# Kernel tuning notes

Measured on AMD Instinct MI355X. Metric: run time of the kernel, lower is better.

## Reference

```python
import jax, jax.numpy as jnp
import numpy as np

NUM_EMB = 8192
EMB_DIM = 512
SPAN = 8            # max_span == fixed_segment_size
COMMIT = 0.25
BOUND_W = 0.01


def setup_inputs() -> dict:
    key = jax.random.key(0)
    k_x, k_e, k_w = jax.random.split(key, 3)
    B, T, D = 16, 8192, EMB_DIM
    x = jax.random.normal(k_x, (B, T, D), dtype=jnp.float32)
    emb = jax.random.normal(k_e, (NUM_EMB, D), dtype=jnp.float32) * 0.02
    Wb = jax.random.normal(k_w, (D, 1), dtype=jnp.float32) * 0.02
    bb = jnp.zeros((1,), dtype=jnp.float32)
    return {"x": x, "emb": emb, "Wb": Wb, "bb": bb}


def reference(x, emb, Wb, bb):
    # Eval-mode forward of AdaptiveTemporalVQ (no gumbel sampling, no EMA update).
    B, T, D = x.shape
    # boundary predictor: Linear(D, 1) -> squeeze
    boundary_logits = (x @ Wb)[..., 0] + bb[0]                      # [B, T]
    boundaries = (jax.nn.sigmoid(boundary_logits) > 0.5).astype(x.dtype)

    num_segments = (T + SPAN - 1) // SPAN
    pad = num_segments * SPAN - T
    x_p = jnp.pad(x, ((0, 0), (0, pad), (0, 0))) if pad > 0 else x
    # temporal mean pooling over fixed segments
    pooled = x_p.reshape(B, num_segments, SPAN, D).mean(axis=2)      # [B, S, D]

    # --- VectorQuantizer ---
    flat = pooled.reshape(-1, D)                                     # [N, D]
    dist = (jnp.sum(flat ** 2, axis=1, keepdims=True)
            + jnp.sum(emb ** 2, axis=1)
            - 2.0 * flat @ emb.T)                                    # [N, K]
    idx = jnp.argmin(dist, axis=1)                                   # [N]
    quantized = emb[idx].reshape(B, num_segments, D)                 # codebook gather

    e_latent_loss = jnp.mean((jax.lax.stop_gradient(quantized) - pooled) ** 2)
    vq_loss = COMMIT * e_latent_loss
    # straight-through estimator
    q_st = pooled + jax.lax.stop_gradient(quantized - pooled)

    # expand each segment code back over its SPAN timesteps
    q_exp = jnp.broadcast_to(q_st[:, :, None, :], (B, num_segments, SPAN, D))
    quantized_out = q_exp.reshape(B, num_segments * SPAN, D)[:, :T, :]
    idx_seg = idx.reshape(B, num_segments)
    idx_out = jnp.broadcast_to(idx_seg[:, :, None], (B, num_segments, SPAN))
    idx_out = idx_out.reshape(B, num_segments * SPAN)[:, :T]

    target_rate = jnp.float32(1.0 / SPAN)
    boundary_loss = (boundaries.mean() - target_rate) ** 2
    total_loss = vq_loss + BOUND_W * boundary_loss
    return quantized_out, total_loss, idx_out, boundaries
```

## Files before the change

### kernel.cpp

```cpp
#include <hip/hip_runtime.h>

#define B_    16
#define T_    8192
#define D_    512
#define K_    8192
#define S_    1024
#define N_    16384
#define NBT   131072

#define LOSS_OFF 67108864
#define IDX_OFF  67108865
#define BND_OFF  67239937

typedef __bf16 bf16x8 __attribute__((ext_vector_type(8)));
typedef float  f32x4  __attribute__((ext_vector_type(4)));

__device__ __forceinline__ unsigned int fsort(float f){
  unsigned int u = __float_as_uint(f);
  return (u & 0x80000000u) ? ~u : (u | 0x80000000u);
}
__device__ __forceinline__ float funsort(unsigned int su){
  unsigned int u = (su & 0x80000000u) ? (su ^ 0x80000000u) : ~su;
  return __uint_as_float(u);
}
__device__ __forceinline__ unsigned short f2bf(float f){
  unsigned int u = __float_as_uint(f);
  return (unsigned short)((u + 0x7fffu + ((u >> 16) & 1u)) >> 16);
}
__device__ __forceinline__ void gload16(const void* g, void* l){
  __builtin_amdgcn_global_load_lds((const __attribute__((address_space(1))) void*)g,
                                   (__attribute__((address_space(3))) void*)l, 16, 0, 0);
}

#define VMW8()  asm volatile("s_waitcnt vmcnt(8)")
#define VMW4()  asm volatile("s_waitcnt vmcnt(4)")
#define VMW0()  asm volatile("s_waitcnt vmcnt(0)")
#define LGKW()  asm volatile("s_waitcnt lgkmcnt(0)")
#define DSR(dst, addr, OFF) \
  asm volatile("ds_read_b128 %0, %1 offset:" OFF : "=&v"(dst) : "v"(addr))

__global__ void k_embnorm(const float4* __restrict__ emb4, float* __restrict__ enorm,
                          unsigned short* __restrict__ embh, int* __restrict__ cnt){
  if(blockIdx.x == 0 && threadIdx.x == 0) *cnt = 0;
  const int wid  = (blockIdx.x * blockDim.x + threadIdx.x) >> 6;
  const int lane = threadIdx.x & 63;
  float4 a = emb4[wid * 128 + (lane << 1)];
  float4 b = emb4[wid * 128 + (lane << 1) + 1];
  float s = a.x*a.x + a.y*a.y + a.z*a.z + a.w*a.w
          + b.x*b.x + b.y*b.y + b.z*b.z + b.w*b.w;
  #pragma unroll
  for(int off = 32; off; off >>= 1) s += __shfl_xor(s, off);
  if(lane == 0) enorm[wid] = s;
  unsigned short* dst = embh + ((size_t)wid << 9) + (lane << 3);
  *(ushort4*)(dst)     = make_ushort4(f2bf(a.x), f2bf(a.y), f2bf(a.z), f2bf(a.w));
  *(ushort4*)(dst + 4) = make_ushort4(f2bf(b.x), f2bf(b.y), f2bf(b.z), f2bf(b.w));
}

__launch_bounds__(256)
__global__ void k_prep(const float4* __restrict__ x4, const float4* __restrict__ wb4,
                       const float* __restrict__ bb, float4* __restrict__ pooled4,
                       unsigned short* __restrict__ pooledh, float* __restrict__ bnd,
                       int* __restrict__ cnt){
  __shared__ double ld[4][8][8];
  const int tid  = threadIdx.x;
  const int row0 = blockIdx.x << 5;
  const double bbv = (double)bb[0];
  #pragma unroll
  for(int it = 0; it < 2; it++){
    const int slot  = (it << 8) + tid;
    const int seg_l = slot >> 7;
    const int c4    = slot & 127;
    const float4 w  = wb4[c4];
    const float4* src = x4 + ((size_t)(row0 + (seg_l << 3)) * 128 + c4);
    float4 acc = src[0];
    double p[8];
    p[0] = (double)acc.x*w.x + (double)acc.y*w.y + (double)acc.z*w.z + (double)acc.w*w.w;
    #pragma unroll
    for(int t = 1; t < 8; t++){
      const float4 v = src[(size_t)t * 128];
      acc.x += v.x; acc.y += v.y; acc.z += v.z; acc.w += v.w;
      p[t] = (double)v.x*w.x + (double)v.y*w.y + (double)v.z*w.z + (double)v.w*w.w;
    }
    acc.x *= 0.125f; acc.y *= 0.125f; acc.z *= 0.125f; acc.w *= 0.125f;
    const int u = ((blockIdx.x << 2) + seg_l) * 128 + c4;
    pooled4[u] = acc;
    *(ushort4*)(pooledh + ((size_t)u << 2)) =
        make_ushort4(f2bf(acc.x), f2bf(acc.y), f2bf(acc.z), f2bf(acc.w));
    #pragma unroll
    for(int t = 0; t < 8; t++){
      #pragma unroll
      for(int off = 1; off < 16; off <<= 1) p[t] += __shfl_xor(p[t], off);
    }
    if((c4 & 15) == 0){
      #pragma unroll
      for(int t = 0; t < 8; t++) ld[seg_l][t][c4 >> 4] = p[t];
    }
  }
  __syncthreads();
  if(tid < 32){
    const double* q = ld[tid >> 3][tid & 7];
    double s = bbv;
    #pragma unroll
    for(int h = 0; h < 8; h++) s += q[h];
    const bool f = s > 0.0;
    bnd[row0 + tid] = f ? 1.0f : 0.0f;
    const unsigned long long m = __ballot(f);
    if(tid == 0) atomicAdd(cnt, (int)__popcll(m));
  }
}

__launch_bounds__(512, 2)
__global__ void k_distx(const unsigned short* __restrict__ Ah,
                        const unsigned short* __restrict__ Bh,
                        const float* __restrict__ enorm,
                        unsigned long long* __restrict__ cand64){
  __shared__ __align__(16) unsigned short smem[65536];

  const int tid  = threadIdx.x;
  const int w    = tid >> 6, lane = tid & 63;
  const int wm   = w >> 2,  wn   = w & 3;
  const int c    = lane & 15, q  = lane >> 4;

  const int bid   = blockIdx.x;
  const int xcd   = bid & 7;
  const int local = bid >> 3;
  const int row_t = (xcd << 3) + (local & 7);
  const int col_t = local >> 3;
  const int rowbase = row_t << 8;
  const int colbase = col_t << 8;

  f32x4 acc[8][4];
  #pragma unroll
  for(int i = 0; i < 8; i++)
    #pragma unroll
    for(int j = 0; j < 4; j++) acc[i][j] = (f32x4){0.f, 0.f, 0.f, 0.f};

  const int sr  = tid >> 2;
  const int cg  = (((tid & 3) ^ ((tid >> 3) & 3)) << 3);
  const int wbase = w << 9;

  const unsigned short* As0 = Ah + (size_t)(rowbase + sr)       * 512 + cg;
  const unsigned short* As1 = Ah + (size_t)(rowbase + 128 + sr) * 512 + cg;
  const unsigned short* Bs0 = Bh + (size_t)(colbase + sr)       * 512 + cg;
  const unsigned short* Bs1 = Bh + (size_t)(colbase + 128 + sr) * 512 + cg;

  const int chb = ((q ^ ((c >> 1) & 3)) << 4);
  const int abA = (wm*128 + c)*64 + chb;
  const int abB = 16384 + (wn*64 + c)*64 + chb;

  bf16x8 af[4], bg[4];

  #define SA(tt) do{ const int sb_ = ((tt) & 3) << 14; const size_t ko_ = (size_t)(tt) << 5; \
    gload16(As0 + ko_, &smem[sb_ + wbase]);                                                  \
    gload16(As1 + ko_, &smem[sb_ + 4096  + wbase]); }while(0)
  #define SB(tt) do{ const int sb_ = ((tt) & 3) << 14; const size_t ko_ = (size_t)(tt) << 5; \
    gload16(Bs0 + ko_, &smem[sb_ + 8192  + wbase]);                                          \
    gload16(Bs1 + ko_, &smem[sb_ + 12288 + wbase]); }while(0)

  #define PHASE_A(tt, DOST) do{                                             \
    const int la_ = ((tt) & 3) << 15;                                       \
    const int vA_ = abA + la_;                                              \
    const int vB_ = abB + la_;                                              \
    DSR(bg[0], vB_, "0");    DSR(bg[1], vB_, "1024");                       \
    DSR(bg[2], vB_, "2048"); DSR(bg[3], vB_, "3072");                       \
    DSR(af[0], vA_, "0");    DSR(af[1], vA_, "1024");                       \
    DSR(af[2], vA_, "2048"); DSR(af[3], vA_, "3072");                       \
    if(DOST) SA((tt) + 3);                                                  \
    __builtin_amdgcn_s_barrier();                                           \
    LGKW();                                                                 \
    __builtin_amdgcn_sched_barrier(0);                                      \
    __builtin_amdgcn_s_setprio(1);                                          \
    _Pragma("unroll")                                                       \
    for(int i = 0; i < 4; i++)                                              \
      _Pragma("unroll")                                                     \
      for(int j = 0; j < 4; j++)                                            \
        acc[i][j] = __builtin_amdgcn_mfma_f32_16x16x32_bf16(af[i], bg[j], acc[i][j], 0, 0, 0); \
    __builtin_amdgcn_s_setprio(0);                                          \
    __builtin_amdgcn_s_barrier();                                           \
  }while(0)

  #define PHASE_B(tt, DOST) do{                                             \
    const int la_ = ((tt) & 3) << 15;                                       \
    const int vA_ = abA + la_;                                              \
    DSR(af[0], vA_, "4096"); DSR(af[1], vA_, "5120");                       \
    DSR(af[2], vA_, "6144"); DSR(af[3], vA_, "7168");                       \
    if(DOST) SB((tt) + 3);                                                  \
    __builtin_amdgcn_s_barrier();                                           \
    LGKW();                                                                 \
    __builtin_amdgcn_sched_barrier(0);                                      \
    __builtin_amdgcn_s_setprio(1);                                          \
    _Pragma("unroll")                                                       \
    for(int i = 0; i < 4; i++)                                              \
      _Pragma("unroll")                                                     \
      for(int j = 0; j < 4; j++)                                            \
        acc[i+4][j] = __builtin_amdgcn_mfma_f32_16x16x32_bf16(af[i], bg[j], acc[i+4][j], 0, 0, 0); \
    __builtin_amdgcn_s_setprio(0);                                          \
  }while(0)

  SA(0); SB(0); SA(1); SB(1); SA(2); SB(2);
  VMW8();
  __builtin_amdgcn_s_barrier();

  #pragma unroll 1
  for(int t = 0; t < 13; ++t){
    PHASE_A(t, 1);
    PHASE_B(t, 1);
    VMW8();
    __builtin_amdgcn_s_barrier();
  }
  PHASE_A(13, 0); PHASE_B(13, 0); VMW4(); __builtin_amdgcn_s_barrier();
  PHASE_A(14, 0); PHASE_B(14, 0); VMW0(); __builtin_amdgcn_s_barrier();
  PHASE_A(15, 0); PHASE_B(15, 0);

  #undef SA
  #undef SB
  #undef PHASE_A
  #undef PHASE_B

  float en[4];
  #pragma unroll
  for(int j = 0; j < 4; j++) en[j] = enorm[colbase + wn*64 + j*16 + c];

  #pragma unroll
  for(int i = 0; i < 8; i++){
    #pragma unroll
    for(int r = 0; r < 4; r++){
      unsigned int k1 = 0xffffffffu, k2 = 0xffffffffu;
      #pragma unroll
      for(int j = 0; j < 4; j++){
        const float d = fmaf(-2.0f, acc[i][j][r], en[j]);
        const unsigned int col = (unsigned int)(colbase + wn*64 + j*16 + c);
        const unsigned int key = (fsort(d) & 0xffffe000u) | col;
        if(key < k1){ k2 = k1; k1 = key; } else if(key < k2){ k2 = key; }
      }
      #pragma unroll
      for(int off = 1; off < 16; off <<= 1){
        const unsigned int o1 = __shfl_xor(k1, off);
        const unsigned int o2 = __shfl_xor(k2, off);
        if(o1 < k1){ k2 = min(k1, o2); k1 = o1; }
        else       { k2 = min(k2, o1); }
      }
      if(c == 0){
        const int row = rowbase + wm*128 + i*16 + (q << 2) + r;
        cand64[((size_t)row << 7) + (col_t << 2) + wn] =
            ((unsigned long long)k2 << 32) | k1;
      }
    }
  }
}

__launch_bounds__(256)
__global__ void k_fixup(const float* __restrict__ pooled, const float* __restrict__ emb,
                        const unsigned long long* __restrict__ cand64,
                        int* __restrict__ idxf, double* __restrict__ part){
  const int lane = threadIdx.x & 63, wv = threadIdx.x >> 6;
  const int row = (blockIdx.x << 2) + wv;
  const ulonglong2* cr = (const ulonglong2*)(cand64 + ((size_t)row << 7));
  const ulonglong2 v = cr[lane];
  unsigned int ks[4];
  ks[0] = (unsigned int)v.x; ks[1] = (unsigned int)(v.x >> 32);
  ks[2] = (unsigned int)v.y; ks[3] = (unsigned int)(v.y >> 32);
  unsigned int mn = min(min(ks[0], ks[1]), min(ks[2], ks[3]));
  #pragma unroll
  for(int off = 32; off; off >>= 1) mn = min(mn, (unsigned int)__shfl_xor(mn, off));
  const float thr = funsort(mn & 0xffffe000u) + 0.01f;

  double bestd = 1e300; int besti = 0x7fffffff;
  const float4* p4 = (const float4*)(pooled + ((size_t)row << 9));
  const float4 pa = p4[lane << 1], pb = p4[(lane << 1) + 1];
  #pragma unroll
  for(int g = 0; g < 4; g++){
    const bool flag = funsort(ks[g] & 0xffffe000u) <= thr;
    unsigned long long mask = __ballot(flag);
    while(mask){
      const int l = __ffsll(mask) - 1;
      mask &= mask - 1;
      const int code = (int)(__shfl(ks[g], l) & 0x1fffu);
      const float4* e4 = (const float4*)(emb + ((size_t)code << 9));
      const float4 ea = e4[lane << 1], eb = e4[(lane << 1) + 1];
      double s = 0.0, d;
      d = (double)pa.x - ea.x; s += d * d;  d = (double)pa.y - ea.y; s += d * d;
      d = (double)pa.z - ea.z; s += d * d;  d = (double)pa.w - ea.w; s += d * d;
      d = (double)pb.x - eb.x; s += d * d;  d = (double)pb.y - eb.y; s += d * d;
      d = (double)pb.z - eb.z; s += d * d;  d = (double)pb.w - eb.w; s += d * d;
      #pragma unroll
      for(int off = 32; off; off >>= 1) s += __shfl_xor(s, off);
      if(s < bestd || (s == bestd && code < besti)){ bestd = s; besti = code; }
    }
  }
  __shared__ double se[4];
  if(lane == 0){ idxf[row] = besti; se[wv] = bestd; }
  __syncthreads();
  if(threadIdx.x == 0) part[blockIdx.x] = se[0] + se[1] + se[2] + se[3];
}

__global__ void k_loss(const double* __restrict__ part, const int* __restrict__ cnt,
                       float* __restrict__ out_loss){
  const int tid = threadIdx.x;
  double s = 0.0;
  for(int i = tid; i < 4096; i += 256) s += part[i];
  #pragma unroll
  for(int off = 32; off; off >>= 1) s += __shfl_xor(s, off);
  __shared__ double sb[4];
  if((tid & 63) == 0) sb[tid >> 6] = s;
  __syncthreads();
  if(tid == 0){
    const double e  = sb[0] + sb[1] + sb[2] + sb[3];
    const double el = e / (double)((size_t)N_ * 512);
    const double bm = (double)(*cnt) / 131072.0 - 0.125;
    const double loss = 0.25 * el + 0.01 * bm * bm;
    *out_loss = (float)loss;
  }
}

__launch_bounds__(256)
__global__ void k_expand(const float4* __restrict__ emb4, const int* __restrict__ idxf,
                         float4* __restrict__ q4, float* __restrict__ idxo){
  const int lane = threadIdx.x & 63, wv = threadIdx.x >> 6;
  const int seg = (blockIdx.x << 2) + wv;
  const int idx = idxf[seg];
  const float4 a = emb4[idx * 128 + (lane << 1)];
  const float4 b = emb4[idx * 128 + (lane << 1) + 1];
  float4* dst = q4 + ((size_t)seg << 10);
  #pragma unroll
  for(int t = 0; t < 8; t++){
    dst[t * 128 + (lane << 1)]     = a;
    dst[t * 128 + (lane << 1) + 1] = b;
  }
  if(lane < 8) idxo[(seg << 3) + lane] = (float)idx;
}

extern "C" void kernel_launch(void* const* d_in, const int* in_sizes, int n_in,
                              void* d_out, int out_size, void* d_ws, size_t ws_size,
                              hipStream_t stream){
  const float* x   = (const float*)d_in[0];
  const float* emb = (const float*)d_in[1];
  const float* wb  = (const float*)d_in[2];
  const float* bb  = (const float*)d_in[3];
  float* out = (float*)d_out;

  char* ws = (char*)d_ws;
  int*    cnt   = (int*)(ws + 0);
  double* part  = (double*)(ws + 64);
  float*  enorm = (float*)(ws + 32832);
  int*    idxf  = (int*)(ws + 65600);

  float*              pooled  = (float*)d_out;
  unsigned long long* cand64  = (unsigned long long*)((char*)d_out + (48ull  << 20));
  unsigned short*     pooledh = (unsigned short*)((char*)d_out + (80ull  << 20));
  unsigned short*     embh    = (unsigned short*)((char*)d_out + (100ull << 20));

  float* bnd   = out + BND_OFF;
  float* idxo  = out + IDX_OFF;
  float* lossp = out + LOSS_OFF;

  hipLaunchKernelGGL(k_embnorm, dim3(2048),  dim3(256), 0, stream, (const float4*)emb, enorm, embh, cnt);
  hipLaunchKernelGGL(k_prep,    dim3(4096),  dim3(256), 0, stream, (const float4*)x, (const float4*)wb,
                     bb, (float4*)pooled, pooledh, bnd, cnt);
  hipLaunchKernelGGL(k_distx,   dim3(2048),  dim3(512), 0, stream, pooledh, embh, enorm, cand64);
  hipLaunchKernelGGL(k_fixup,   dim3(4096),  dim3(256), 0, stream, pooled, emb, cand64, idxf, part);
  hipLaunchKernelGGL(k_loss,    dim3(1),     dim3(256), 0, stream, part, cnt, lossp);
  hipLaunchKernelGGL(k_expand,  dim3(4096),  dim3(256), 0, stream, (const float4*)emb, idxf, (float4*)d_out, idxo);
}
```

Before: 709.7 us.

## Double-buffer LDS fragment registers to overlap ds_reads with MFMA in GEMM loop

Restructures the distance GEMM main loop so the next K-tile's B and first-half A fragments are read from LDS into a second register set while the current tile's MFMAs run. Partial lgkmcnt waits replace full waits, and one barrier per phase is dropped. This aims to hide LDS read latency behind matrix math, at the cost of more fragment registers (possible occupancy or spill pressure) and finer wait-count reasoning that must match the stage rotation.

```diff
diff --git a/kernel.cpp b/kernel.cpp
--- a/kernel.cpp
+++ b/kernel.cpp
@@ -32,10 +32,12 @@
                                    (__attribute__((address_space(3))) void*)l, 16, 0, 0);
 }
 
-#define VMW8()  asm volatile("s_waitcnt vmcnt(8)")
-#define VMW4()  asm volatile("s_waitcnt vmcnt(4)")
-#define VMW0()  asm volatile("s_waitcnt vmcnt(0)")
-#define LGKW()  asm volatile("s_waitcnt lgkmcnt(0)")
+#define WAITLGK(n) asm volatile("s_waitcnt lgkmcnt(" #n ")")
+#define WAITVM(n)  asm volatile("s_waitcnt vmcnt(" #n ")")
+#define SBAR()     __builtin_amdgcn_s_barrier()
+#define SCHED0()   __builtin_amdgcn_sched_barrier(0)
+#define SETP1()    __builtin_amdgcn_s_setprio(1)
+#define SETP0()    __builtin_amdgcn_s_setprio(0)
 #define DSR(dst, addr, OFF) \
   asm volatile("ds_read_b128 %0, %1 offset:" OFF : "=&v"(dst) : "v"(addr))
 
@@ -148,7 +150,7 @@
   const int abA = (wm*128 + c)*64 + chb;
   const int abB = 16384 + (wn*64 + c)*64 + chb;
 
-  bf16x8 af[4], bg[4];
+  bf16x8 bgr[2][4], afr[2][4], afb[4];
 
   #define SA(tt) do{ const int sb_ = ((tt) & 3) << 14; const size_t ko_ = (size_t)(tt) << 5; \
     gload16(As0 + ko_, &smem[sb_ + wbase]);                                                  \
@@ -157,65 +159,79 @@
     gload16(Bs0 + ko_, &smem[sb_ + 8192  + wbase]);                                          \
     gload16(Bs1 + ko_, &smem[sb_ + 12288 + wbase]); }while(0)
 
-  #define PHASE_A(tt, DOST) do{                                             \
-    const int la_ = ((tt) & 3) << 15;                                       \
-    const int vA_ = abA + la_;                                              \
-    const int vB_ = abB + la_;                                              \
-    DSR(bg[0], vB_, "0");    DSR(bg[1], vB_, "1024");                       \
-    DSR(bg[2], vB_, "2048"); DSR(bg[3], vB_, "3072");                       \
-    DSR(af[0], vA_, "0");    DSR(af[1], vA_, "1024");                       \
-    DSR(af[2], vA_, "2048"); DSR(af[3], vA_, "3072");                       \
-    if(DOST) SA((tt) + 3);                                                  \
-    __builtin_amdgcn_s_barrier();                                           \
-    LGKW();                                                                 \
-    __builtin_amdgcn_sched_barrier(0);                                      \
-    __builtin_amdgcn_s_setprio(1);                                          \
-    _Pragma("unroll")                                                       \
-    for(int i = 0; i < 4; i++)                                              \
-      _Pragma("unroll")                                                     \
-      for(int j = 0; j < 4; j++)                                            \
-        acc[i][j] = __builtin_amdgcn_mfma_f32_16x16x32_bf16(af[i], bg[j], acc[i][j], 0, 0, 0); \
-    __builtin_amdgcn_s_setprio(0);                                          \
-    __builtin_amdgcn_s_barrier();                                           \
-  }while(0)
-
-  #define PHASE_B(tt, DOST) do{                                             \
-    const int la_ = ((tt) & 3) << 15;                                       \
-    const int vA_ = abA + la_;                                              \
-    DSR(af[0], vA_, "4096"); DSR(af[1], vA_, "5120");                       \
-    DSR(af[2], vA_, "6144"); DSR(af[3], vA_, "7168");                       \
-    if(DOST) SB((tt) + 3);                                                  \
-    __builtin_amdgcn_s_barrier();                                           \
-    LGKW();                                                                 \
-    __builtin_amdgcn_sched_barrier(0);                                      \
-    __builtin_amdgcn_s_setprio(1);                                          \
-    _Pragma("unroll")                                                       \
-    for(int i = 0; i < 4; i++)                                              \
-      _Pragma("unroll")                                                     \
-      for(int j = 0; j < 4; j++)                                            \
-        acc[i+4][j] = __builtin_amdgcn_mfma_f32_16x16x32_bf16(af[i], bg[j], acc[i+4][j], 0, 0, 0); \
-    __builtin_amdgcn_s_setprio(0);                                          \
+  #define DSR8(st, BUF) do{                                       \
+    const int vB_ = abB + (BUF);                                  \
+    const int vA_ = abA + (BUF);                                  \
+    DSR(bgr[st][0], vB_, "0");    DSR(bgr[st][1], vB_, "1024");   \
+    DSR(bgr[st][2], vB_, "2048"); DSR(bgr[st][3], vB_, "3072");   \
+    DSR(afr[st][0], vA_, "0");    DSR(afr[st][1], vA_, "1024");   \
+    DSR(afr[st][2], vA_, "2048"); DSR(afr[st][3], vA_, "3072");   \
+  }while(0)
+
+  #define DSR4(BUF) do{                                           \
+    const int vA_ = abA + (BUF);                                  \
+    DSR(afb[0], vA_, "4096"); DSR(afb[1], vA_, "5120");           \
+    DSR(afb[2], vA_, "6144"); DSR(afb[3], vA_, "7168");           \
+  }while(0)
+
+  #define MFMA16_A(st) do{ _Pragma("unroll")                                  \
+    for(int i = 0; i < 4; i++) _Pragma("unroll")                              \
+      for(int j = 0; j < 4; j++)                                              \
+        acc[i][j] = __builtin_amdgcn_mfma_f32_16x16x32_bf16(                  \
+            afr[st][i], bgr[st][j], acc[i][j], 0, 0, 0); }while(0)
+  #define MFMA16_B(st) do{ _Pragma("unroll")                                  \
+    for(int i = 0; i < 4; i++) _Pragma("unroll")                              \
+      for(int j = 0; j < 4; j++)                                              \
+        acc[i+4][j] = __builtin_amdgcn_mfma_f32_16x16x32_bf16(                \
+            afb[i], bgr[st][j], acc[i+4][j], 0, 0, 0); }while(0)
+
+  #define PH_A(t_, st, DOST, VMN) do{               \
+    DSR4(((t_) & 3) << 15);                         \
+    if(DOST) SA((t_) + 3);                          \
+    WAITLGK(4); SCHED0();                           \
+    SETP1(); MFMA16_A(st); SETP0();                 \
+    WAITVM(VMN);                                    \
+    SBAR();                                         \
+  }while(0)
+
+  #define PH_B(t_, st, DOST) do{                    \
+    DSR8(1 - (st), (((t_) + 1) & 3) << 15);         \
+    if(DOST) SB((t_) + 3);                          \
+    WAITLGK(8); SCHED0();                           \
+    SETP1(); MFMA16_B(st); SETP0();                 \
+    SBAR();                                         \
+  }while(0)
+
+  #define PH_B_LAST(st) do{                         \
+    WAITLGK(0); SCHED0();                           \
+    SETP1(); MFMA16_B(st); SETP0();                 \
   }while(0)
 
   SA(0); SB(0); SA(1); SB(1); SA(2); SB(2);
-  VMW8();
-  __builtin_amdgcn_s_barrier();
+  WAITVM(8);
+  SBAR();
+  DSR8(0, 0);
 
   #pragma unroll 1
-  for(int t = 0; t < 13; ++t){
-    PHASE_A(t, 1);
-    PHASE_B(t, 1);
-    VMW8();
-    __builtin_amdgcn_s_barrier();
-  }
-  PHASE_A(13, 0); PHASE_B(13, 0); VMW4(); __builtin_amdgcn_s_barrier();
-  PHASE_A(14, 0); PHASE_B(14, 0); VMW0(); __builtin_amdgcn_s_barrier();
-  PHASE_A(15, 0); PHASE_B(15, 0);
+  for(int u = 0; u < 6; ++u){
+    const int t = u << 1;
+    PH_A(t,     0, 1, 6);  PH_B(t,     0, 1);
+    PH_A(t + 1, 1, 1, 6);  PH_B(t + 1, 1, 1);
+  }
+  PH_A(12, 0, 1, 6);  PH_B(12, 0, 1);
+  PH_A(13, 1, 0, 4);  PH_B(13, 1, 0);
+  PH_A(14, 0, 0, 0);  PH_B(14, 0, 0);
+  PH_A(15, 1, 0, 0);  PH_B_LAST(1);
 
   #undef SA
   #undef SB
-  #undef PHASE_A
-  #undef PHASE_B
+  #undef DSR8
+  #undef DSR4
+  #undef MFMA16_A
+  #undef MFMA16_B
+  #undef PH_A
+  #undef PH_B
+  #undef PH_B_LAST
 
   float en[4];
   #pragma unroll
```

Result: no change. 701.3 us (-1.2%).
